# Optimization experiments

Measured on AMD Instinct MI355X. Metric: run time of the kernel, lower is better.

## Reference

```python
import jax, jax.numpy as jnp
import numpy as np

N_HEADS = 12
B, S, D = 2, 2048, 768
NEG = -1e9


def setup_inputs() -> dict:
    key = jax.random.key(0)
    ks = jax.random.split(key, 7)
    scale = 1.0 / np.sqrt(D)
    Q = jax.random.normal(ks[0], (B, S, D), jnp.float32)
    K = jax.random.normal(ks[1], (B, S, D), jnp.float32)
    V = jax.random.normal(ks[2], (B, S, D), jnp.float32)
    # causal mask, broadcastable over batch and heads; 0 entries are masked out
    mask = jnp.tril(jnp.ones((S, S), jnp.int32))[None, None, :, :]
    Wq = jax.random.normal(ks[3], (D, D), jnp.float32) * scale
    Wk = jax.random.normal(ks[4], (D, D), jnp.float32) * scale
    Wv = jax.random.normal(ks[5], (D, D), jnp.float32) * scale
    Wo = jax.random.normal(ks[6], (D, D), jnp.float32) * scale
    return {"Q": Q, "K": K, "V": V, "mask": mask,
            "Wq": Wq, "Wk": Wk, "Wv": Wv, "Wo": Wo}


def reference(Q, K, V, mask, Wq, Wk, Wv, Wo):
    b, s, d = Q.shape
    h = N_HEADS
    dk = d // h
    # projections (torch nn.Linear: x @ W.T), split heads -> (b, h, s, dk)
    q = (Q @ Wq.T).reshape(b, s, h, dk).transpose(0, 2, 1, 3)
    k = (K @ Wk.T).reshape(b, s, h, dk).transpose(0, 2, 1, 3)
    v = (V @ Wv.T).reshape(b, s, h, dk).transpose(0, 2, 1, 3)
    scores = jnp.einsum('bhqd,bhkd->bhqk', q, k) / jnp.sqrt(jnp.asarray(dk, q.dtype))
    scores = jnp.where(mask == 0, jnp.asarray(NEG, scores.dtype), scores)
    attn = jax.nn.softmax(scores, axis=-1)  # dropout p=0.0 -> identity
    ctx = jnp.einsum('bhqk,bhkd->bhqd', attn, v)
    ctx = ctx.transpose(0, 2, 1, 3).reshape(b, s, d)
    return ctx @ Wo.T
```

## Files before the change

### kernel.cpp

```cpp
#include <hip/hip_runtime.h>
#include <math.h>

#define NH     12
#define BB     2
#define SEQ    2048
#define DMODEL 768
#define DK     64

typedef __attribute__((ext_vector_type(8))) short short8;
typedef __attribute__((ext_vector_type(4))) short short4v;
typedef __attribute__((ext_vector_type(4))) float floatx4;

__device__ __forceinline__ unsigned short f2bf(float x) {
    unsigned u = __builtin_bit_cast(unsigned, x);
    u = (u + 0x7fffu + ((u >> 16) & 1u)) >> 16;
    return (unsigned short)u;
}
__device__ __forceinline__ unsigned short f2bf_fast(float x) {
    unsigned u = __builtin_bit_cast(unsigned, x);
    return (unsigned short)((u + 0x8000u) >> 16);
}

__device__ __forceinline__ void gld_lds16(const ushort* gptr, ushort* lptr) {
    __builtin_amdgcn_global_load_lds(
        (const __attribute__((address_space(1))) unsigned int*)(const void*)gptr,
        (__attribute__((address_space(3))) unsigned int*)(void*)lptr,
        16, 0, 0);
}

__device__ __forceinline__ short4v shfl8(short4v v, int src) {
    int2 t = __builtin_bit_cast(int2, v);
    t.x = __shfl(t.x, src);
    t.y = __shfl(t.y, src);
    return __builtin_bit_cast(short4v, t);
}

#define SI (BB * SEQ * DMODEL)
#define SW (DMODEL * DMODEL)

__global__ __launch_bounds__(256) void cast_w(
    const float* __restrict__ Wq, const float* __restrict__ Wk,
    const float* __restrict__ Wv, const float* __restrict__ Wo,
    ushort* oWq, ushort* oWk, ushort* oWv, ushort* oWo, int* counter) {
    if (blockIdx.x == 0 && threadIdx.x == 0) *counter = 0;
    long i = (long)(blockIdx.x * 256 + threadIdx.x) * 4;
    const float* src; ushort* dst; long off;
    if      (i < 1L * SW) { src = Wq; dst = oWq; off = i; }
    else if (i < 2L * SW) { src = Wk; dst = oWk; off = i - 1L * SW; }
    else if (i < 3L * SW) { src = Wv; dst = oWv; off = i - 2L * SW; }
    else                  { src = Wo; dst = oWo; off = i - 3L * SW; }
    float4 v = *(const float4*)(src + off);
    ushort4 o;
    o.x = f2bf(v.x); o.y = f2bf(v.y); o.z = f2bf(v.z); o.w = f2bf(v.w);
    *(ushort4*)(dst + off) = o;
}

template<int MODE, bool AF32>
__device__ __forceinline__ void gemm_body(const void* __restrict__ Av,
                                          const ushort* __restrict__ W,
                                          float* __restrict__ outF,
                                          ushort* __restrict__ outH,
                                          float scale) {
    const int n0 = blockIdx.x * 128;
    const int m0 = blockIdx.y * 128;
    const int tid  = threadIdx.x;
    const int lane = tid & 63;
    const int wv   = tid >> 6;
    const int l15  = lane & 15;
    const int quad = lane >> 4;
    const int wm = (wv >> 1) * 64;
    const int wn = (wv & 1) * 64;

    __shared__ __align__(16) ushort S[2][2][128 * 32];

    const int srow = tid >> 2;
    const int sch  = tid & 3;
    const int schx = sch ^ ((srow >> 1) & 3);
    const int sw2  = (l15 >> 1) & 3;

    const ushort* Ab = (const ushort*)Av;
    const float*  Af = (const float*)Av;

    floatx4 acc[4][4];
    #pragma unroll
    for (int i = 0; i < 4; ++i)
        #pragma unroll
        for (int j = 0; j < 4; ++j) acc[i][j] = (floatx4)0.f;

    float4 ar0[2], ar1[2];
    #pragma unroll
    for (int it = 0; it < 2; ++it) {
        const int r = srow + it * 64;
        if (AF32) {
            const float* p = Af + (size_t)(m0 + r) * DMODEL + schx * 8;
            ar0[it] = *(const float4*)p;
            ar1[it] = *(const float4*)(p + 4);
        } else {
            gld_lds16(Ab + (size_t)(m0 + r) * DMODEL + schx * 8, &S[0][0][r * 32 + sch * 8]);
        }
        gld_lds16(W + (size_t)(n0 + r) * DMODEL + schx * 8, &S[0][1][r * 32 + sch * 8]);
    }
    if (AF32) {
        #pragma unroll
        for (int it = 0; it < 2; ++it) {
            const int r = srow + it * 64;
            short8 s8;
            s8[0] = (short)f2bf(ar0[it].x); s8[1] = (short)f2bf(ar0[it].y);
            s8[2] = (short)f2bf(ar0[it].z); s8[3] = (short)f2bf(ar0[it].w);
            s8[4] = (short)f2bf(ar1[it].x); s8[5] = (short)f2bf(ar1[it].y);
            s8[6] = (short)f2bf(ar1[it].z); s8[7] = (short)f2bf(ar1[it].w);
            *(short8*)&S[0][0][r * 32 + sch * 8] = s8;
        }
    }

    const int NS = DMODEL / 32;
    for (int t = 0; t < NS; ++t) {
        __syncthreads();
        const int bi = (t + 1) & 1;
        if (t + 1 < NS) {
            const int k0 = (t + 1) * 32;
            #pragma unroll
            for (int it = 0; it < 2; ++it) {
                const int r = srow + it * 64;
                if (AF32) {
                    const float* p = Af + (size_t)(m0 + r) * DMODEL + k0 + schx * 8;
                    ar0[it] = *(const float4*)p;
                    ar1[it] = *(const float4*)(p + 4);
                } else {
                    gld_lds16(Ab + (size_t)(m0 + r) * DMODEL + k0 + schx * 8, &S[bi][0][r * 32 + sch * 8]);
                }
                gld_lds16(W + (size_t)(n0 + r) * DMODEL + k0 + schx * 8, &S[bi][1][r * 32 + sch * 8]);
            }
        }
        const ushort* As  = S[t & 1][0];
        const ushort* Ws2 = S[t & 1][1];
        short8 af[4], bf[4];
        #pragma unroll
        for (int mi = 0; mi < 4; ++mi)
            af[mi] = *(const short8*)&As[(wm + mi * 16 + l15) * 32 + ((quad ^ sw2) * 8)];
        #pragma unroll
        for (int ni = 0; ni < 4; ++ni)
            bf[ni] = *(const short8*)&Ws2[(wn + ni * 16 + l15) * 32 + ((quad ^ sw2) * 8)];
        #pragma unroll
        for (int mi = 0; mi < 4; ++mi)
            #pragma unroll
            for (int ni = 0; ni < 4; ++ni) {
                if (MODE == 2)
                    acc[mi][ni] = __builtin_amdgcn_mfma_f32_16x16x32_bf16(bf[ni], af[mi], acc[mi][ni], 0, 0, 0);
                else
                    acc[mi][ni] = __builtin_amdgcn_mfma_f32_16x16x32_bf16(af[mi], bf[ni], acc[mi][ni], 0, 0, 0);
            }
        if (AF32 && t + 1 < NS) {
            #pragma unroll
            for (int it = 0; it < 2; ++it) {
                const int r = srow + it * 64;
                short8 s8;
                s8[0] = (short)f2bf(ar0[it].x); s8[1] = (short)f2bf(ar0[it].y);
                s8[2] = (short)f2bf(ar0[it].z); s8[3] = (short)f2bf(ar0[it].w);
                s8[4] = (short)f2bf(ar1[it].x); s8[5] = (short)f2bf(ar1[it].y);
                s8[6] = (short)f2bf(ar1[it].z); s8[7] = (short)f2bf(ar1[it].w);
                *(short8*)&S[bi][0][r * 32 + sch * 8] = s8;
            }
        }
    }

    #pragma unroll
    for (int mi = 0; mi < 4; ++mi)
        #pragma unroll
        for (int ni = 0; ni < 4; ++ni)
            #pragma unroll
            for (int r = 0; r < 4; ++r) {
                const float v = acc[mi][ni][r] * scale;
                if (MODE == 2) {
                    const int m = m0 + wm + mi * 16 + l15;
                    const int n = n0 + wn + ni * 16 + quad * 4 + r;
                    const int b = m >> 11, s = m & (SEQ - 1);
                    const int h = n >> 6,  dk = n & 63;
                    outH[(((size_t)b * NH + h) * DK + dk) * SEQ + s] = f2bf(v);
                } else {
                    const int m = m0 + wm + mi * 16 + quad * 4 + r;
                    const int n = n0 + wn + ni * 16 + l15;
                    if (MODE == 0) {
                        outF[(size_t)m * DMODEL + n] = v;
                    } else {
                        const int b = m >> 11, s = m & (SEQ - 1);
                        const int h = n >> 6,  dk = n & 63;
                        outH[(((size_t)b * NH + h) * SEQ + s) * DK + dk] = f2bf(v);
                    }
                }
            }
}

#define QSCALE (0.125f * 1.44269504088896f)

__global__ __launch_bounds__(256) void gemm_qkv(
    const float* Q, const float* K, const float* V,
    const ushort* Wqb, const ushort* Wkb, const ushort* Wvb,
    ushort* qh, ushort* kh, ushort* vhT) {
    const int z = blockIdx.z;
    if (z == 0)      gemm_body<1, true>(Q, Wqb, nullptr, qh,  QSCALE);
    else if (z == 1) gemm_body<1, true>(K, Wkb, nullptr, kh,  1.0f);
    else             gemm_body<2, true>(V, Wvb, nullptr, vhT, 1.0f);
}

__global__ __launch_bounds__(256) void gemm_out(const ushort* A, const ushort* W, float* out) {
    gemm_body<0, false>(A, W, out, nullptr, 1.0f);
}

#define NITEMS (24 * 32)
#define MBIAS  -20.0f

__global__ __launch_bounds__(256) void flash_mfma(const ushort* __restrict__ qh,
                                                  const ushort* __restrict__ kh,
                                                  const ushort* __restrict__ vhT,
                                                  ushort* __restrict__ ctx,
                                                  int* __restrict__ counter) {
    const int tid  = threadIdx.x;
    const int lane = tid & 63;
    const int wv   = tid >> 6;
    const int l15  = lane & 15;
    const int quad = lane >> 4;

    __shared__ __align__(16) ushort KV[3][2][64 * 64];
    __shared__ int wshare;

    const int srow = tid >> 3;
    const int sch  = tid & 7;
    const int schx = sch ^ (srow & 7);
    const int swq  = l15 & 7;

    const int srcA = l15 + 32 * (quad & 1);
    const int srcB = srcA + 16;
    const bool hiq = (quad >> 1) != 0;

    for (;;) {
        if (tid == 0) wshare = atomicAdd(counter, 1);
        __syncthreads();
        const int w = wshare;
        if (w >= NITEMS) break;
        const int qt = 31 - (w / 24);
        const int bh = w - (w / 24) * 24;
        const int b  = bh / NH, h = bh % NH;
        const int q0 = qt * 64;

        const ushort* kbase = kh  + (size_t)bh * SEQ * DK;
        const ushort* vbase = vhT + (size_t)bh * DK * SEQ;

        short8 q_frag[2];
        {
            const ushort* qp_ = qh + ((size_t)bh * SEQ + q0 + wv * 16 + l15) * DK;
            q_frag[0] = *(const short8*)(qp_ + quad * 8);
            q_frag[1] = *(const short8*)(qp_ + 32 + quad * 8);
        }

        gld_lds16(kbase + (size_t)srow * DK + schx * 8,         &KV[0][0][srow * 64 + sch * 8]);
        gld_lds16(kbase + (size_t)(srow + 32) * DK + schx * 8,  &KV[0][0][(srow + 32) * 64 + sch * 8]);
        gld_lds16(vbase + (size_t)srow * SEQ + schx * 8,        &KV[0][1][srow * 64 + sch * 8]);
        gld_lds16(vbase + (size_t)(srow + 32) * SEQ + schx * 8, &KV[0][1][(srow + 32) * 64 + sch * 8]);
        if (qt >= 1) {
            gld_lds16(kbase + (size_t)(64 + srow) * DK + schx * 8,      &KV[1][0][srow * 64 + sch * 8]);
            gld_lds16(kbase + (size_t)(64 + srow + 32) * DK + schx * 8, &KV[1][0][(srow + 32) * 64 + sch * 8]);
            gld_lds16(vbase + (size_t)srow * SEQ + 64 + schx * 8,       &KV[1][1][srow * 64 + sch * 8]);
            gld_lds16(vbase + (size_t)(srow + 32) * SEQ + 64 + schx * 8,&KV[1][1][(srow + 32) * 64 + sch * 8]);
        }

        float l_s = 0.f;
        floatx4 o_acc[4];
        #pragma unroll
        for (int d = 0; d < 4; ++d) o_acc[d] = (floatx4)0.f;

        for (int kt = 0; kt <= qt; ++kt) {
            if (kt < qt) {
                asm volatile("s_waitcnt vmcnt(4)\n\ts_barrier" ::: "memory");
            } else {
                asm volatile("s_waitcnt vmcnt(0)\n\ts_barrier" ::: "memory");
            }
            if (kt + 2 <= qt) {
                const int k0 = (kt + 2) * 64;
                const int bi = (kt + 2) % 3;
                gld_lds16(kbase + (size_t)(k0 + srow) * DK + schx * 8,        &KV[bi][0][srow * 64 + sch * 8]);
                gld_lds16(kbase + (size_t)(k0 + srow + 32) * DK + schx * 8,   &KV[bi][0][(srow + 32) * 64 + sch * 8]);
                gld_lds16(vbase + (size_t)srow * SEQ + k0 + schx * 8,         &KV[bi][1][srow * 64 + sch * 8]);
                gld_lds16(vbase + (size_t)(srow + 32) * SEQ + k0 + schx * 8,  &KV[bi][1][(srow + 32) * 64 + sch * 8]);
            }
            const int cb = kt % 3;
            const ushort* Ks  = KV[cb][0];
            const ushort* Vts = KV[cb][1];

            floatx4 s_acc[4];
            #pragma unroll
            for (int nt = 0; nt < 4; ++nt) s_acc[nt] = (floatx4)(MBIAS);
            #pragma unroll
            for (int kc = 0; kc < 2; ++kc)
                #pragma unroll
                for (int nt = 0; nt < 4; ++nt) {
                    short8 kf = *(const short8*)&Ks[(nt * 16 + l15) * 64 + (((kc * 4 + quad) ^ swq) * 8)];
                    s_acc[nt] = __builtin_amdgcn_mfma_f32_16x16x32_bf16(kf, q_frag[kc], s_acc[nt], 0, 0, 0);
                }

            if (kt == qt) {
                const int ql = wv * 16 + l15;
                #pragma unroll
                for (int nt = 0; nt < 4; ++nt)
                    #pragma unroll
                    for (int r = 0; r < 4; ++r)
                        if (nt * 16 + quad * 4 + r > ql) s_acc[nt][r] = -1.0e30f;
            }

            short4v packed[4];
            #pragma unroll
            for (int nt = 0; nt < 4; ++nt)
                #pragma unroll
                for (int r = 0; r < 4; ++r) {
                    const float p = exp2f(s_acc[nt][r]);
                    l_s += p;
                    packed[nt][r] = (short)f2bf_fast(p);
                }

            #pragma unroll
            for (int kc = 0; kc < 2; ++kc) {
                short4v a0 = shfl8(packed[2 * kc],     srcA);
                short4v a1 = shfl8(packed[2 * kc + 1], srcA);
                short4v b0 = shfl8(packed[2 * kc],     srcB);
                short4v b1 = shfl8(packed[2 * kc + 1], srcB);
                short4v lo = hiq ? a1 : a0;
                short4v hi = hiq ? b1 : b0;
                short8 pf;
                pf[0] = lo[0]; pf[1] = lo[1]; pf[2] = lo[2]; pf[3] = lo[3];
                pf[4] = hi[0]; pf[5] = hi[1]; pf[6] = hi[2]; pf[7] = hi[3];
                #pragma unroll
                for (int dkt = 0; dkt < 4; ++dkt) {
                    short8 vf = *(const short8*)&Vts[(dkt * 16 + l15) * 64 + (((kc * 4 + quad) ^ swq) * 8)];
                    o_acc[dkt] = __builtin_amdgcn_mfma_f32_16x16x32_bf16(pf, vf, o_acc[dkt], 0, 0, 0);
                }
            }
        }

        l_s += __shfl_xor(l_s, 16);
        l_s += __shfl_xor(l_s, 32);

        #pragma unroll
        for (int r = 0; r < 4; ++r) {
            const float lr = __shfl(l_s, quad * 20 + r);
            const float inv = 1.f / lr;
            const int s = q0 + wv * 16 + quad * 4 + r;
            #pragma unroll
            for (int dkt = 0; dkt < 4; ++dkt) {
                const int d = h * DK + dkt * 16 + l15;
                ctx[((size_t)b * SEQ + s) * DMODEL + d] = f2bf(o_acc[dkt][r] * inv);
            }
        }
    }
}

extern "C" void kernel_launch(void* const* d_in, const int* in_sizes, int n_in,
                              void* d_out, int out_size, void* d_ws, size_t ws_size,
                              hipStream_t stream) {
    const float* Q  = (const float*)d_in[0];
    const float* K  = (const float*)d_in[1];
    const float* V  = (const float*)d_in[2];
    const float* Wq = (const float*)d_in[4];
    const float* Wk = (const float*)d_in[5];
    const float* Wv = (const float*)d_in[6];
    const float* Wo = (const float*)d_in[7];

    char* ws = (char*)d_ws;
    const size_t SZ_IN = (size_t)SI * 2;
    const size_t SZ_W  = (size_t)SW * 2;
    ushort* Wqb = (ushort*)(ws);
    ushort* Wkb = (ushort*)(ws + SZ_W);
    ushort* Wvb = (ushort*)(ws + 2 * SZ_W);
    ushort* Wob = (ushort*)(ws + 3 * SZ_W);
    ushort* qh  = (ushort*)(ws + 4 * SZ_W);
    ushort* kh  = (ushort*)(ws + 4 * SZ_W + SZ_IN);
    ushort* vhT = (ushort*)(ws + 4 * SZ_W + 2 * SZ_IN);
    ushort* ctx = (ushort*)(ws + 4 * SZ_W + 3 * SZ_IN);
    int*    ctr = (int*)   (ws + 4 * SZ_W + 4 * SZ_IN);

    dim3 blk(256);
    cast_w<<<dim3(4 * SW / 1024), blk, 0, stream>>>(Wq, Wk, Wv, Wo,
                                                    Wqb, Wkb, Wvb, Wob, ctr);
    gemm_qkv<<<dim3(6, 32, 3), blk, 0, stream>>>(Q, K, V, Wqb, Wkb, Wvb, qh, kh, vhT);
    flash_mfma<<<dim3(768), blk, 0, stream>>>(qh, kh, vhT, ctx, ctr);
    gemm_out<<<dim3(6, 32), blk, 0, stream>>>(ctx, Wob, (float*)d_out);
}
```

Measured before the change: 239.6 us.

## Split causal attention into split-K chunks with separate combine kernel

Measured after the change: 234.5 us. -2.2%, faster.

```diff
diff --git a/kernel.cpp b/kernel.cpp
--- a/kernel.cpp
+++ b/kernel.cpp
@@ -19,6 +19,10 @@
 __device__ __forceinline__ unsigned short f2bf_fast(float x) {
     unsigned u = __builtin_bit_cast(unsigned, x);
     return (unsigned short)((u + 0x8000u) >> 16);
+}
+__device__ __forceinline__ float bf2f(unsigned short h) {
+    unsigned u = ((unsigned)h) << 16;
+    return __builtin_bit_cast(float, u);
 }
 
 __device__ __forceinline__ void gld_lds16(const ushort* gptr, ushort* lptr) {
@@ -105,10 +109,10 @@
         for (int it = 0; it < 2; ++it) {
             const int r = srow + it * 64;
             short8 s8;
-            s8[0] = (short)f2bf(ar0[it].x); s8[1] = (short)f2bf(ar0[it].y);
-            s8[2] = (short)f2bf(ar0[it].z); s8[3] = (short)f2bf(ar0[it].w);
-            s8[4] = (short)f2bf(ar1[it].x); s8[5] = (short)f2bf(ar1[it].y);
-            s8[6] = (short)f2bf(ar1[it].z); s8[7] = (short)f2bf(ar1[it].w);
+            s8[0] = (short)f2bf_fast(ar0[it].x); s8[1] = (short)f2bf_fast(ar0[it].y);
+            s8[2] = (short)f2bf_fast(ar0[it].z); s8[3] = (short)f2bf_fast(ar0[it].w);
+            s8[4] = (short)f2bf_fast(ar1[it].x); s8[5] = (short)f2bf_fast(ar1[it].y);
+            s8[6] = (short)f2bf_fast(ar1[it].z); s8[7] = (short)f2bf_fast(ar1[it].w);
             *(short8*)&S[0][0][r * 32 + sch * 8] = s8;
         }
     }
@@ -155,10 +159,10 @@
             for (int it = 0; it < 2; ++it) {
                 const int r = srow + it * 64;
                 short8 s8;
-                s8[0] = (short)f2bf(ar0[it].x); s8[1] = (short)f2bf(ar0[it].y);
-                s8[2] = (short)f2bf(ar0[it].z); s8[3] = (short)f2bf(ar0[it].w);
-                s8[4] = (short)f2bf(ar1[it].x); s8[5] = (short)f2bf(ar1[it].y);
-                s8[6] = (short)f2bf(ar1[it].z); s8[7] = (short)f2bf(ar1[it].w);
+                s8[0] = (short)f2bf_fast(ar0[it].x); s8[1] = (short)f2bf_fast(ar0[it].y);
+                s8[2] = (short)f2bf_fast(ar0[it].z); s8[3] = (short)f2bf_fast(ar0[it].w);
+                s8[4] = (short)f2bf_fast(ar1[it].x); s8[5] = (short)f2bf_fast(ar1[it].y);
+                s8[6] = (short)f2bf_fast(ar1[it].z); s8[7] = (short)f2bf_fast(ar1[it].w);
                 *(short8*)&S[bi][0][r * 32 + sch * 8] = s8;
             }
         }
@@ -207,21 +211,24 @@
     gemm_body<0, false>(A, W, out, nullptr, 1.0f);
 }
 
-#define NITEMS (24 * 32)
-#define MBIAS  -20.0f
-
-__global__ __launch_bounds__(256) void flash_mfma(const ushort* __restrict__ qh,
-                                                  const ushort* __restrict__ kh,
-                                                  const ushort* __restrict__ vhT,
-                                                  ushort* __restrict__ ctx,
-                                                  int* __restrict__ counter) {
+#define NIT   (24 * 72)
+#define MBIAS -20.0f
+__device__ const int d_offs[17] = {0,1,2,4,6,9,12,16,20,25,30,36,42,49,56,64,72};
+
+__global__ __launch_bounds__(256, 4) void flash_p1(const ushort* __restrict__ qh,
+                                                   const ushort* __restrict__ kh,
+                                                   const ushort* __restrict__ vhT,
+                                                   ushort* __restrict__ ctx,
+                                                   ushort* __restrict__ Opart,
+                                                   float* __restrict__ lpart,
+                                                   int* __restrict__ counter) {
     const int tid  = threadIdx.x;
     const int lane = tid & 63;
     const int wv   = tid >> 6;
     const int l15  = lane & 15;
     const int quad = lane >> 4;
 
-    __shared__ __align__(16) ushort KV[3][2][64 * 64];
+    __shared__ __align__(16) ushort KV[2][2][64 * 64];
     __shared__ int wshare;
 
     const int srow = tid >> 3;
@@ -237,119 +244,186 @@
         if (tid == 0) wshare = atomicAdd(counter, 1);
         __syncthreads();
         const int w = wshare;
-        if (w >= NITEMS) break;
-        const int qt = 31 - (w / 24);
-        const int bh = w - (w / 24) * 24;
+        if (w >= NIT) break;
+        const int bh = w / 72;
+        const int r72 = w - bh * 72;
+        int Q = 0;
+        #pragma unroll
+        for (int q = 0; q < 16; ++q) if (r72 >= d_offs[q + 1]) Q = q + 1;
+        const int s  = r72 - d_offs[Q];
+        const int ns = (Q >> 1) + 1;
         const int b  = bh / NH, h = bh % NH;
-        const int q0 = qt * 64;
+        const int qbase = Q * 128;
+        const int k_lo = 4 * s;
+        const int k_hi = min(4 * s + 3, 2 * Q + 1);
 
         const ushort* kbase = kh  + (size_t)bh * SEQ * DK;
         const ushort* vbase = vhT + (size_t)bh * DK * SEQ;
 
-        short8 q_frag[2];
+        short8 qf[2][2];
+        #pragma unroll
+        for (int qs = 0; qs < 2; ++qs) {
+            const ushort* qp = qh + ((size_t)bh * SEQ + qbase + wv * 32 + qs * 16 + l15) * DK;
+            qf[qs][0] = *(const short8*)(qp + quad * 8);
+            qf[qs][1] = *(const short8*)(qp + 32 + quad * 8);
+        }
+
         {
-            const ushort* qp_ = qh + ((size_t)bh * SEQ + q0 + wv * 16 + l15) * DK;
-            q_frag[0] = *(const short8*)(qp_ + quad * 8);
-            q_frag[1] = *(const short8*)(qp_ + 32 + quad * 8);
-        }
-
-        gld_lds16(kbase + (size_t)srow * DK + schx * 8,         &KV[0][0][srow * 64 + sch * 8]);
-        gld_lds16(kbase + (size_t)(srow + 32) * DK + schx * 8,  &KV[0][0][(srow + 32) * 64 + sch * 8]);
-        gld_lds16(vbase + (size_t)srow * SEQ + schx * 8,        &KV[0][1][srow * 64 + sch * 8]);
-        gld_lds16(vbase + (size_t)(srow + 32) * SEQ + schx * 8, &KV[0][1][(srow + 32) * 64 + sch * 8]);
-        if (qt >= 1) {
-            gld_lds16(kbase + (size_t)(64 + srow) * DK + schx * 8,      &KV[1][0][srow * 64 + sch * 8]);
-            gld_lds16(kbase + (size_t)(64 + srow + 32) * DK + schx * 8, &KV[1][0][(srow + 32) * 64 + sch * 8]);
-            gld_lds16(vbase + (size_t)srow * SEQ + 64 + schx * 8,       &KV[1][1][srow * 64 + sch * 8]);
-            gld_lds16(vbase + (size_t)(srow + 32) * SEQ + 64 + schx * 8,&KV[1][1][(srow + 32) * 64 + sch * 8]);
-        }
-
-        float l_s = 0.f;
-        floatx4 o_acc[4];
-        #pragma unroll
-        for (int d = 0; d < 4; ++d) o_acc[d] = (floatx4)0.f;
-
-        for (int kt = 0; kt <= qt; ++kt) {
-            if (kt < qt) {
-                asm volatile("s_waitcnt vmcnt(4)\n\ts_barrier" ::: "memory");
-            } else {
-                asm volatile("s_waitcnt vmcnt(0)\n\ts_barrier" ::: "memory");
-            }
-            if (kt + 2 <= qt) {
-                const int k0 = (kt + 2) * 64;
-                const int bi = (kt + 2) % 3;
+            const int k0 = k_lo * 64;
+            gld_lds16(kbase + (size_t)(k0 + srow) * DK + schx * 8,        &KV[0][0][srow * 64 + sch * 8]);
+            gld_lds16(kbase + (size_t)(k0 + srow + 32) * DK + schx * 8,   &KV[0][0][(srow + 32) * 64 + sch * 8]);
+            gld_lds16(vbase + (size_t)srow * SEQ + k0 + schx * 8,         &KV[0][1][srow * 64 + sch * 8]);
+            gld_lds16(vbase + (size_t)(srow + 32) * SEQ + k0 + schx * 8,  &KV[0][1][(srow + 32) * 64 + sch * 8]);
+        }
+
+        float l_s[2] = {0.f, 0.f};
+        floatx4 o_acc[2][4];
+        #pragma unroll
+        for (int qs = 0; qs < 2; ++qs)
+            #pragma unroll
+            for (int d = 0; d < 4; ++d) o_acc[qs][d] = (floatx4)0.f;
+
+        for (int kt = k_lo; kt <= k_hi; ++kt) {
+            __syncthreads();
+            if (kt < k_hi) {
+                const int k0 = (kt + 1) * 64;
+                const int bi = (kt + 1 - k_lo) & 1;
                 gld_lds16(kbase + (size_t)(k0 + srow) * DK + schx * 8,        &KV[bi][0][srow * 64 + sch * 8]);
                 gld_lds16(kbase + (size_t)(k0 + srow + 32) * DK + schx * 8,   &KV[bi][0][(srow + 32) * 64 + sch * 8]);
                 gld_lds16(vbase + (size_t)srow * SEQ + k0 + schx * 8,         &KV[bi][1][srow * 64 + sch * 8]);
                 gld_lds16(vbase + (size_t)(srow + 32) * SEQ + k0 + schx * 8,  &KV[bi][1][(srow + 32) * 64 + sch * 8]);
             }
-            const int cb = kt % 3;
+            const int cb = (kt - k_lo) & 1;
             const ushort* Ks  = KV[cb][0];
             const ushort* Vts = KV[cb][1];
-
-            floatx4 s_acc[4];
-            #pragma unroll
-            for (int nt = 0; nt < 4; ++nt) s_acc[nt] = (floatx4)(MBIAS);
-            #pragma unroll
-            for (int kc = 0; kc < 2; ++kc)
-                #pragma unroll
-                for (int nt = 0; nt < 4; ++nt) {
-                    short8 kf = *(const short8*)&Ks[(nt * 16 + l15) * 64 + (((kc * 4 + quad) ^ swq) * 8)];
-                    s_acc[nt] = __builtin_amdgcn_mfma_f32_16x16x32_bf16(kf, q_frag[kc], s_acc[nt], 0, 0, 0);
-                }
-
-            if (kt == qt) {
-                const int ql = wv * 16 + l15;
+            const bool diag = (kt >= 2 * Q);
+
+            #pragma unroll
+            for (int qs = 0; qs < 2; ++qs) {
+                floatx4 s_acc[4];
+                #pragma unroll
+                for (int nt = 0; nt < 4; ++nt) s_acc[nt] = (floatx4)(MBIAS);
+                #pragma unroll
+                for (int kc = 0; kc < 2; ++kc)
+                    #pragma unroll
+                    for (int nt = 0; nt < 4; ++nt) {
+                        short8 kf = *(const short8*)&Ks[(nt * 16 + l15) * 64 + (((kc * 4 + quad) ^ swq) * 8)];
+                        s_acc[nt] = __builtin_amdgcn_mfma_f32_16x16x32_bf16(kf, qf[qs][kc], s_acc[nt], 0, 0, 0);
+                    }
+
+                if (diag) {
+                    const int qg = qbase + wv * 32 + qs * 16 + l15;
+                    #pragma unroll
+                    for (int nt = 0; nt < 4; ++nt)
+                        #pragma unroll
+                        for (int rr = 0; rr < 4; ++rr)
+                            if (kt * 64 + nt * 16 + quad * 4 + rr > qg) s_acc[nt][rr] = -1.0e30f;
+                }
+
+                short4v packed[4];
                 #pragma unroll
                 for (int nt = 0; nt < 4; ++nt)
                     #pragma unroll
-                    for (int r = 0; r < 4; ++r)
-                        if (nt * 16 + quad * 4 + r > ql) s_acc[nt][r] = -1.0e30f;
-            }
-
-            short4v packed[4];
-            #pragma unroll
-            for (int nt = 0; nt < 4; ++nt)
-                #pragma unroll
-                for (int r = 0; r < 4; ++r) {
-                    const float p = exp2f(s_acc[nt][r]);
-                    l_s += p;
-                    packed[nt][r] = (short)f2bf_fast(p);
-                }
-
-            #pragma unroll
-            for (int kc = 0; kc < 2; ++kc) {
-                short4v a0 = shfl8(packed[2 * kc],     srcA);
-                short4v a1 = shfl8(packed[2 * kc + 1], srcA);
-                short4v b0 = shfl8(packed[2 * kc],     srcB);
-                short4v b1 = shfl8(packed[2 * kc + 1], srcB);
-                short4v lo = hiq ? a1 : a0;
-                short4v hi = hiq ? b1 : b0;
-                short8 pf;
-                pf[0] = lo[0]; pf[1] = lo[1]; pf[2] = lo[2]; pf[3] = lo[3];
-                pf[4] = hi[0]; pf[5] = hi[1]; pf[6] = hi[2]; pf[7] = hi[3];
-                #pragma unroll
-                for (int dkt = 0; dkt < 4; ++dkt) {
-                    short8 vf = *(const short8*)&Vts[(dkt * 16 + l15) * 64 + (((kc * 4 + quad) ^ swq) * 8)];
-                    o_acc[dkt] = __builtin_amdgcn_mfma_f32_16x16x32_bf16(pf, vf, o_acc[dkt], 0, 0, 0);
-                }
-            }
-        }
-
-        l_s += __shfl_xor(l_s, 16);
-        l_s += __shfl_xor(l_s, 32);
-
-        #pragma unroll
-        for (int r = 0; r < 4; ++r) {
-            const float lr = __shfl(l_s, quad * 20 + r);
-            const float inv = 1.f / lr;
-            const int s = q0 + wv * 16 + quad * 4 + r;
-            #pragma unroll
-            for (int dkt = 0; dkt < 4; ++dkt) {
-                const int d = h * DK + dkt * 16 + l15;
-                ctx[((size_t)b * SEQ + s) * DMODEL + d] = f2bf(o_acc[dkt][r] * inv);
-            }
-        }
+                    for (int rr = 0; rr < 4; ++rr) {
+                        const float p = exp2f(s_acc[nt][rr]);
+                        l_s[qs] += p;
+                        packed[nt][rr] = (short)f2bf_fast(p);
+                    }
+
+                #pragma unroll
+                for (int kc = 0; kc < 2; ++kc) {
+                    short4v a0 = shfl8(packed[2 * kc],     srcA);
+                    short4v a1 = shfl8(packed[2 * kc + 1], srcA);
+                    short4v b0 = shfl8(packed[2 * kc],     srcB);
+                    short4v b1 = shfl8(packed[2 * kc + 1], srcB);
+                    short4v lo = hiq ? a1 : a0;
+                    short4v hi = hiq ? b1 : b0;
+                    short8 pf;
+                    pf[0] = lo[0]; pf[1] = lo[1]; pf[2] = lo[2]; pf[3] = lo[3];
+                    pf[4] = hi[0]; pf[5] = hi[1]; pf[6] = hi[2]; pf[7] = hi[3];
+                    #pragma unroll
+                    for (int dkt = 0; dkt < 4; ++dkt) {
+                        short8 vf = *(const short8*)&Vts[(dkt * 16 + l15) * 64 + (((kc * 4 + quad) ^ swq) * 8)];
+                        o_acc[qs][dkt] = __builtin_amdgcn_mfma_f32_16x16x32_bf16(pf, vf, o_acc[qs][dkt], 0, 0, 0);
+                    }
+                }
+            }
+        }
+
+        #pragma unroll
+        for (int qs = 0; qs < 2; ++qs) {
+            l_s[qs] += __shfl_xor(l_s[qs], 16);
+            l_s[qs] += __shfl_xor(l_s[qs], 32);
+        }
+
+        if (ns == 1) {
+            #pragma unroll
+            for (int qs = 0; qs < 2; ++qs)
+                #pragma unroll
+                for (int rr = 0; rr < 4; ++rr) {
+                    const float lr = __shfl(l_s[qs], quad * 20 + rr);
+                    const float inv = 1.f / lr;
+                    const int sg = qbase + wv * 32 + qs * 16 + quad * 4 + rr;
+                    #pragma unroll
+                    for (int dkt = 0; dkt < 4; ++dkt) {
+                        const int d = h * DK + dkt * 16 + l15;
+                        ctx[((size_t)b * SEQ + sg) * DMODEL + d] = f2bf(o_acc[qs][dkt][rr] * inv);
+                    }
+                }
+        } else {
+            const int pid = bh * 70 + (d_offs[Q] - 2) + s;
+            ushort* op = Opart + (size_t)pid * (128 * 64);
+            #pragma unroll
+            for (int qs = 0; qs < 2; ++qs) {
+                #pragma unroll
+                for (int rr = 0; rr < 4; ++rr) {
+                    const int row = wv * 32 + qs * 16 + quad * 4 + rr;
+                    #pragma unroll
+                    for (int dkt = 0; dkt < 4; ++dkt)
+                        op[row * 64 + dkt * 16 + l15] = f2bf(o_acc[qs][dkt][rr]);
+                }
+                if (quad == 0)
+                    lpart[(size_t)pid * 128 + wv * 32 + qs * 16 + l15] = l_s[qs];
+            }
+        }
+    }
+}
+
+__global__ __launch_bounds__(256) void flash_combine(const ushort* __restrict__ Opart,
+                                                     const float* __restrict__ lpart,
+                                                     ushort* __restrict__ ctx) {
+    const int bh = blockIdx.x / 14;
+    const int Q  = 2 + blockIdx.x % 14;
+    const int ns = (Q >> 1) + 1;
+    const int pbase = bh * 70 + (d_offs[Q] - 2);
+    const int b = bh / NH, h = bh % NH;
+    const int t = threadIdx.x;
+    const int row = t >> 1;
+    const int c0  = (t & 1) * 32;
+
+    float lt = 0.f;
+    for (int s2 = 0; s2 < ns; ++s2) lt += lpart[(size_t)(pbase + s2) * 128 + row];
+    const float inv = 1.f / lt;
+
+    float acc[32];
+    #pragma unroll
+    for (int j = 0; j < 32; ++j) acc[j] = 0.f;
+    for (int s2 = 0; s2 < ns; ++s2) {
+        const ushort* op = Opart + (size_t)(pbase + s2) * (128 * 64) + row * 64 + c0;
+        #pragma unroll
+        for (int j = 0; j < 32; j += 8) {
+            short8 v = *(const short8*)(op + j);
+            #pragma unroll
+            for (int e = 0; e < 8; ++e) acc[j + e] += bf2f((unsigned short)v[e]);
+        }
+    }
+    ushort* dst = ctx + ((size_t)b * SEQ + Q * 128 + row) * DMODEL + h * DK + c0;
+    #pragma unroll
+    for (int j = 0; j < 32; j += 8) {
+        short8 o;
+        #pragma unroll
+        for (int e = 0; e < 8; ++e) o[e] = (short)f2bf(acc[j + e] * inv);
+        *(short8*)(dst + j) = o;
     }
 }
 
@@ -367,20 +441,24 @@
     char* ws = (char*)d_ws;
     const size_t SZ_IN = (size_t)SI * 2;
     const size_t SZ_W  = (size_t)SW * 2;
-    ushort* Wqb = (ushort*)(ws);
-    ushort* Wkb = (ushort*)(ws + SZ_W);
-    ushort* Wvb = (ushort*)(ws + 2 * SZ_W);
-    ushort* Wob = (ushort*)(ws + 3 * SZ_W);
-    ushort* qh  = (ushort*)(ws + 4 * SZ_W);
-    ushort* kh  = (ushort*)(ws + 4 * SZ_W + SZ_IN);
-    ushort* vhT = (ushort*)(ws + 4 * SZ_W + 2 * SZ_IN);
-    ushort* ctx = (ushort*)(ws + 4 * SZ_W + 3 * SZ_IN);
-    int*    ctr = (int*)   (ws + 4 * SZ_W + 4 * SZ_IN);
+    ushort* Wqb   = (ushort*)(ws);
+    ushort* Wkb   = (ushort*)(ws + SZ_W);
+    ushort* Wvb   = (ushort*)(ws + 2 * SZ_W);
+    ushort* Wob   = (ushort*)(ws + 3 * SZ_W);
+    ushort* qh    = (ushort*)(ws + 4 * SZ_W);
+    ushort* kh    = (ushort*)(ws + 4 * SZ_W + SZ_IN);
+    ushort* vhT   = (ushort*)(ws + 4 * SZ_W + 2 * SZ_IN);
+    ushort* ctx   = (ushort*)(ws + 4 * SZ_W + 3 * SZ_IN);
+    ushort* Opart = (ushort*)(ws + 4 * SZ_W + 4 * SZ_IN);
+    float*  lpart = (float*) (ws + 4 * SZ_W + 4 * SZ_IN + (size_t)1680 * 8192 * 2);
+    int*    ctr   = (int*)   (ws + 4 * SZ_W + 4 * SZ_IN + (size_t)1680 * 8192 * 2
+                                 + (size_t)1680 * 128 * 4);
 
     dim3 blk(256);
     cast_w<<<dim3(4 * SW / 1024), blk, 0, stream>>>(Wq, Wk, Wv, Wo,
                                                     Wqb, Wkb, Wvb, Wob, ctr);
     gemm_qkv<<<dim3(6, 32, 3), blk, 0, stream>>>(Q, K, V, Wqb, Wkb, Wvb, qh, kh, vhT);
-    flash_mfma<<<dim3(768), blk, 0, stream>>>(qh, kh, vhT, ctx, ctr);
+    flash_p1<<<dim3(768), blk, 0, stream>>>(qh, kh, vhT, ctx, Opart, lpart, ctr);
+    flash_combine<<<dim3(24 * 14), blk, 0, stream>>>(Opart, lpart, ctx);
     gemm_out<<<dim3(6, 32), blk, 0, stream>>>(ctx, Wob, (float*)d_out);
 }
```
